# Kernel optimization log

Measured on AMD Instinct MI355X. Metric: run time of the kernel, lower is better.

## Reference

```python
import jax, jax.numpy as jnp
import numpy as np

B, N, D = 32, 64, 256

def _gelu(x):
    return jax.nn.gelu(x, approximate=False)

def setup_inputs() -> dict:
    key = jax.random.key(0)
    ks = jax.random.split(key, 16)
    def w(k, shape):
        fan_in = shape[0]
        return (jax.random.normal(k, shape, jnp.float32) / np.float32(np.sqrt(fan_in)))
    return {
        "dataset_embedding": jax.random.normal(ks[0], (B, D), jnp.float32),
        "variable_embeddings": jax.random.normal(ks[1], (B, N, D), jnp.float32),
        "claim_context": jax.random.normal(ks[2], (B, D), jnp.float32),
        "dge_w1": w(ks[3], (2 * D, D)), "dge_b1": jnp.zeros((D,), jnp.float32),
        "dge_w2": w(ks[4], (D, D)),     "dge_b2": jnp.zeros((D,), jnp.float32),
        "cge_w1": w(ks[5], (2 * D, D)), "cge_b1": jnp.zeros((D,), jnp.float32),
        "cge_w2": w(ks[6], (D, D)),     "cge_b2": jnp.zeros((D,), jnp.float32),
        "dep_w1": w(ks[7], (4 * D, D)), "dep_b1": jnp.zeros((D,), jnp.float32),
        "dep_w2": w(ks[8], (D, 1)),     "dep_b2": jnp.zeros((1,), jnp.float32),
        "cep_w1": w(ks[9], (4 * D, D)), "cep_b1": jnp.zeros((D,), jnp.float32),
        "cep_w2": w(ks[10], (D, 1)),    "cep_b2": jnp.zeros((1,), jnp.float32),
        "gate_w1": w(ks[11], (3, 64)),  "gate_b1": jnp.zeros((64,), jnp.float32),
        "gate_w2": w(ks[12], (64, 1)),  "gate_b2": jnp.zeros((1,), jnp.float32),
        "n_samples": 500,
    }

def _encode(ve, ctx, w1, b1, w2, b2):
    # Sequential(Linear(2d,d), GELU, Linear(d,d), GELU); dropout=0 (eval)
    x = jnp.concatenate([ve, jnp.broadcast_to(ctx[:, None, :], ve.shape)], axis=-1)
    h = _gelu(x @ w1 + b1)
    return _gelu(h @ w2 + b2)

def _predict_edges(ve_enc, ctx, w1, b1, w2, b2):
    # var_with_context: [B,N,2D]; edge features cat([var_i, var_j]) @ w1
    # == (vwc @ w1[:2D]) broadcast over i + (vwc @ w1[2D:]) broadcast over j
    vwc = jnp.concatenate([ve_enc, jnp.broadcast_to(ctx[:, None, :], ve_enc.shape)], axis=-1)
    wi, wj = w1[: 2 * D], w1[2 * D :]
    fi = vwc @ wi  # [B,N,D]
    fj = vwc @ wj  # [B,N,D]
    h = _gelu(fi[:, :, None, :] + fj[:, None, :, :] + b1)  # [B,N,N,D]
    logits = jnp.einsum("bijd,do->bij", h, w2) + b2[0]
    eye = jnp.eye(N, dtype=bool)
    return jnp.where(eye[None, :, :], jnp.float32(-1e9), logits)

def reference(dataset_embedding, variable_embeddings, claim_context,
              dge_w1, dge_b1, dge_w2, dge_b2,
              cge_w1, cge_b1, cge_w2, cge_b2,
              dep_w1, dep_b1, dep_w2, dep_b2,
              cep_w1, cep_b1, cep_w2, cep_b2,
              gate_w1, gate_b1, gate_w2, gate_b2,
              n_samples):
    avg_claim_confidence = 0.5
    var_data = _encode(variable_embeddings, dataset_embedding, dge_w1, dge_b1, dge_w2, dge_b2)
    var_claim = _encode(variable_embeddings, claim_context, cge_w1, cge_b1, cge_w2, cge_b2)
    W_data_logits = _predict_edges(var_data, dataset_embedding, dep_w1, dep_b1, dep_w2, dep_b2)
    W_claim_logits = _predict_edges(var_claim, claim_context, cep_w1, cep_b1, cep_w2, cep_b2)

    p = jax.nn.sigmoid(W_data_logits)
    eps = jnp.float32(1e-8)
    data_entropy = -(p * jnp.log(p + eps) + (1 - p) * jnp.log(1 - p + eps)).mean(axis=(1, 2))  # [B]

    ns = jnp.full((B,), min(n_samples / 1000.0, 1.0), jnp.float32)
    cc = jnp.full((B,), avg_claim_confidence, jnp.float32)
    gf = jnp.stack([ns, cc, data_entropy], axis=-1)  # [B,3]
    gate = jax.nn.sigmoid(_gelu(gf @ gate_w1 + gate_b1) @ gate_w2 + gate_b2)  # [B,1]
    gate = gate[:, :, None]  # [B,1,1]

    W_post_logits = gate * W_data_logits + (1 - gate) * W_claim_logits

    # NOTEARS: h(W) = tr(expm(W o W)) - n, W = sigmoid(logits)
    Wsig = jax.nn.sigmoid(W_post_logits)
    M = jax.vmap(jax.scipy.linalg.expm)(Wsig * Wsig)
    acyc = (jnp.trace(M, axis1=1, axis2=2) - N).mean()

    W_posterior = jax.nn.sigmoid(W_post_logits)
    return (W_posterior, acyc)
```

## Files before the change

### kernel.cpp

```cpp
#include <hip/hip_runtime.h>
#include <hip/hip_bf16.h>


#define LDS_STRIDE 260
#define ES 68

__device__ __forceinline__ float gelu_f(float x) {
    return 0.5f * x * (1.0f + erff(x * 0.70710678118654752440f));
}
__device__ __forceinline__ float sigmoid_f(float x) {
    return 1.0f / (1.0f + expf(-x));
}
__device__ __forceinline__ float f4c(const float4& v, int k) {
    return k == 0 ? v.x : k == 1 ? v.y : k == 2 ? v.z : v.w;
}
__device__ __forceinline__ float4 ld4(const float* __restrict__ buf, int r, int c) {
    return *(const float4*)&buf[r * ES + c];
}

__global__ __launch_bounds__(256) void k0_ctx(
    const float* __restrict__ ds, const float* __restrict__ cc,
    const float* __restrict__ dge_w1, const float* __restrict__ dge_b1,
    const float* __restrict__ cge_w1, const float* __restrict__ cge_b1,
    const float* __restrict__ dep_w1, const float* __restrict__ dep_b1,
    const float* __restrict__ cep_w1, const float* __restrict__ cep_b1,
    float* __restrict__ ctxproj)
{
    const int b = blockIdx.x;
    const int which = blockIdx.y;
    const float* ctx; const float* W; const float* bias;
    switch (which) {
        case 0:  ctx = ds; W = dge_w1 + 256 * 256; bias = dge_b1; break;
        case 1:  ctx = cc; W = cge_w1 + 256 * 256; bias = cge_b1; break;
        case 2:  ctx = ds; W = dep_w1 + 256 * 256; bias = dep_b1; break;
        case 3:  ctx = ds; W = dep_w1 + 768 * 256; bias = nullptr; break;
        case 4:  ctx = cc; W = cep_w1 + 256 * 256; bias = cep_b1; break;
        default: ctx = cc; W = cep_w1 + 768 * 256; bias = nullptr; break;
    }
    __shared__ float sctx[256];
    const int tid = threadIdx.x;
    sctx[tid] = ctx[b * 256 + tid];
    __syncthreads();
    float acc = 0.0f;
    #pragma unroll 2
    for (int k = 0; k < 256; k += 4) {
        float4 c4 = *(const float4*)&sctx[k];
        acc = fmaf(c4.x, W[(k + 0) * 256 + tid], acc);
        acc = fmaf(c4.y, W[(k + 1) * 256 + tid], acc);
        acc = fmaf(c4.z, W[(k + 2) * 256 + tid], acc);
        acc = fmaf(c4.w, W[(k + 3) * 256 + tid], acc);
    }
    if (bias) acc += bias[tid];
    ctxproj[(which * 32 + b) * 256 + tid] = acc;
}

__device__ __forceinline__ void gemm_ks(const float* __restrict__ src,
                                        const float* __restrict__ W,
                                        int ks0, int t0, float acc[8][4])
{
    #pragma unroll
    for (int r = 0; r < 8; ++r)
        #pragma unroll
        for (int c = 0; c < 4; ++c) acc[r][c] = 0.0f;
    #pragma unroll 2
    for (int k = ks0; k < ks0 + 32; k += 4) {
        float4 wv0 = *(const float4*)&W[(k + 0) * 256 + t0];
        float4 wv1 = *(const float4*)&W[(k + 1) * 256 + t0];
        float4 wv2 = *(const float4*)&W[(k + 2) * 256 + t0];
        float4 wv3 = *(const float4*)&W[(k + 3) * 256 + t0];
        float4 a[8];
        #pragma unroll
        for (int r = 0; r < 8; ++r) a[r] = *(const float4*)&src[r * LDS_STRIDE + k];
        float4 wvs[4] = {wv0, wv1, wv2, wv3};
        #pragma unroll
        for (int kk = 0; kk < 4; ++kk) {
            float4 wv = wvs[kk];
            #pragma unroll
            for (int r = 0; r < 8; ++r) {
                float av = f4c(a[r], kk);
                acc[r][0] = fmaf(av, wv.x, acc[r][0]);
                acc[r][1] = fmaf(av, wv.y, acc[r][1]);
                acc[r][2] = fmaf(av, wv.z, acc[r][2]);
                acc[r][3] = fmaf(av, wv.w, acc[r][3]);
            }
        }
    }
}

__device__ __forceinline__ void write_part(float* __restrict__ part, int w, int t0,
                                           const float acc[8][4])
{
    #pragma unroll
    for (int r = 0; r < 8; ++r) {
        float4 o = {acc[r][0], acc[r][1], acc[r][2], acc[r][3]};
        *(float4*)&part[(w * 8 + r) * 256 + t0] = o;
    }
}

__device__ __forceinline__ float4 reduce_part(const float* __restrict__ part, int r, int t0)
{
    float4 s = {0.0f, 0.0f, 0.0f, 0.0f};
    #pragma unroll
    for (int w = 0; w < 8; ++w) {
        float4 v = *(const float4*)&part[(w * 8 + r) * 256 + t0];
        s.x += v.x; s.y += v.y; s.z += v.z; s.w += v.w;
    }
    return s;
}

__global__ __launch_bounds__(512) void k1_encode(
    const float* __restrict__ ve_g,
    const float* __restrict__ dge_w1, const float* __restrict__ dge_w2, const float* __restrict__ dge_b2,
    const float* __restrict__ cge_w1, const float* __restrict__ cge_w2, const float* __restrict__ cge_b2,
    const float* __restrict__ dep_w1, const float* __restrict__ cep_w1,
    const float* __restrict__ ctxproj,
    float* __restrict__ fi_dep, float* __restrict__ fjt_dep,
    float* __restrict__ fi_cep, float* __restrict__ fjt_cep)
{
    __shared__ float sve[8 * LDS_STRIDE];
    __shared__ float sA[8 * LDS_STRIDE];
    __shared__ float sB[8 * LDS_STRIDE];
    __shared__ float part[8 * 8 * 256];

    const int tid = threadIdx.x;
    const int b = blockIdx.x >> 3;
    const int chunk = blockIdx.x & 7;
    const int n0 = chunk * 8;

    const int w  = tid >> 6;
    const int t0 = (tid & 63) * 4;
    const int ks0 = w * 32;

    {
        int idx = tid * 4;
        int r = idx >> 8, k = idx & 255;
        *(float4*)&sve[r * LDS_STRIDE + k] = *(const float4*)&ve_g[(b * 64 + n0) * 256 + idx];
    }
    __syncthreads();

    float acc[8][4];

    gemm_ks(sve, dge_w1, ks0, t0, acc);
    write_part(part, w, t0, acc);
    __syncthreads();
    {
        float4 s = reduce_part(part, w, t0);
        float4 cp = *(const float4*)&ctxproj[(0 * 32 + b) * 256 + t0];
        float4 o = {gelu_f(s.x + cp.x), gelu_f(s.y + cp.y), gelu_f(s.z + cp.z), gelu_f(s.w + cp.w)};
        *(float4*)&sA[w * LDS_STRIDE + t0] = o;
    }
    __syncthreads();

    gemm_ks(sA, dge_w2, ks0, t0, acc);
    write_part(part, w, t0, acc);
    __syncthreads();
    {
        float4 s = reduce_part(part, w, t0);
        float4 bv = *(const float4*)&dge_b2[t0];
        float4 o = {gelu_f(s.x + bv.x), gelu_f(s.y + bv.y), gelu_f(s.z + bv.z), gelu_f(s.w + bv.w)};
        *(float4*)&sB[w * LDS_STRIDE + t0] = o;
    }
    __syncthreads();

    gemm_ks(sB, dep_w1, ks0, t0, acc);
    write_part(part, w, t0, acc);
    __syncthreads();
    {
        float4 s = reduce_part(part, w, t0);
        float4 cp = *(const float4*)&ctxproj[(2 * 32 + b) * 256 + t0];
        float4 o = {s.x + cp.x, s.y + cp.y, s.z + cp.z, s.w + cp.w};
        *(float4*)&fi_dep[(b * 64 + n0 + w) * 256 + t0] = o;
    }
    __syncthreads();

    gemm_ks(sB, dep_w1 + 512 * 256, ks0, t0, acc);
    write_part(part, w, t0, acc);
    __syncthreads();
    {
        float4 s = reduce_part(part, w, t0);
        float4 cp = *(const float4*)&ctxproj[(3 * 32 + b) * 256 + t0];
        float4 o = {s.x + cp.x, s.y + cp.y, s.z + cp.z, s.w + cp.w};
        *(float4*)&sA[w * LDS_STRIDE + t0] = o;
    }
    __syncthreads();
    {
        int t = tid & 255, half = tid >> 8;
        float v0 = sA[(half * 4 + 0) * LDS_STRIDE + t];
        float v1 = sA[(half * 4 + 1) * LDS_STRIDE + t];
        float v2 = sA[(half * 4 + 2) * LDS_STRIDE + t];
        float v3 = sA[(half * 4 + 3) * LDS_STRIDE + t];
        float4 o = {v0, v1, v2, v3};
        *(float4*)&fjt_dep[(b * 256 + t) * 64 + n0 + half * 4] = o;
    }

    gemm_ks(sve, cge_w1, ks0, t0, acc);
    write_part(part, w, t0, acc);
    __syncthreads();
    {
        float4 s = reduce_part(part, w, t0);
        float4 cp = *(const float4*)&ctxproj[(1 * 32 + b) * 256 + t0];
        float4 o = {gelu_f(s.x + cp.x), gelu_f(s.y + cp.y), gelu_f(s.z + cp.z), gelu_f(s.w + cp.w)};
        *(float4*)&sB[w * LDS_STRIDE + t0] = o;
    }
    __syncthreads();

    gemm_ks(sB, cge_w2, ks0, t0, acc);
    write_part(part, w, t0, acc);
    __syncthreads();
    {
        float4 s = reduce_part(part, w, t0);
        float4 bv = *(const float4*)&cge_b2[t0];
        float4 o = {gelu_f(s.x + bv.x), gelu_f(s.y + bv.y), gelu_f(s.z + bv.z), gelu_f(s.w + bv.w)};
        *(float4*)&sA[w * LDS_STRIDE + t0] = o;
    }
    __syncthreads();

    gemm_ks(sA, cep_w1, ks0, t0, acc);
    write_part(part, w, t0, acc);
    __syncthreads();
    {
        float4 s = reduce_part(part, w, t0);
        float4 cp = *(const float4*)&ctxproj[(4 * 32 + b) * 256 + t0];
        float4 o = {s.x + cp.x, s.y + cp.y, s.z + cp.z, s.w + cp.w};
        *(float4*)&fi_cep[(b * 64 + n0 + w) * 256 + t0] = o;
    }
    __syncthreads();

    gemm_ks(sA, cep_w1 + 512 * 256, ks0, t0, acc);
    write_part(part, w, t0, acc);
    __syncthreads();
    {
        float4 s = reduce_part(part, w, t0);
        float4 cp = *(const float4*)&ctxproj[(5 * 32 + b) * 256 + t0];
        float4 o = {s.x + cp.x, s.y + cp.y, s.z + cp.z, s.w + cp.w};
        *(float4*)&sB[w * LDS_STRIDE + t0] = o;
    }
    __syncthreads();
    {
        int t = tid & 255, half = tid >> 8;
        float v0 = sB[(half * 4 + 0) * LDS_STRIDE + t];
        float v1 = sB[(half * 4 + 1) * LDS_STRIDE + t];
        float v2 = sB[(half * 4 + 2) * LDS_STRIDE + t];
        float v3 = sB[(half * 4 + 3) * LDS_STRIDE + t];
        float4 o = {v0, v1, v2, v3};
        *(float4*)&fjt_cep[(b * 256 + t) * 64 + n0 + half * 4] = o;
    }
}

__global__ __launch_bounds__(256) void k3_edges(
    const float* __restrict__ fi_dep, const float* __restrict__ fjt_dep,
    const float* __restrict__ fi_cep, const float* __restrict__ fjt_cep,
    const float* __restrict__ dep_w2, const float* __restrict__ dep_b2,
    const float* __restrict__ cep_w2, const float* __restrict__ cep_b2,
    float* __restrict__ Wd, float* __restrict__ Wc, float* __restrict__ entp)
{
    __shared__ float fjD_s[64 * 64];
    __shared__ float fjC_s[64 * 64];
    __shared__ float fiD_s[4][256];
    __shared__ float fiC_s[4][256];
    __shared__ float w2D_s[256];
    __shared__ float w2C_s[256];

    const int b   = blockIdx.x >> 4;
    const int ig  = blockIdx.x & 15;
    const int tid = threadIdx.x;
    const int s   = tid >> 6;
    const int j   = tid & 63;
    const int i   = ig * 4 + s;

    {
        int c = j * 4;
        *(float4*)&fiD_s[s][c] = *(const float4*)&fi_dep[(b * 64 + i) * 256 + c];
        *(float4*)&fiC_s[s][c] = *(const float4*)&fi_cep[(b * 64 + i) * 256 + c];
        if (tid < 64) {
            *(float4*)&w2D_s[tid * 4] = *(const float4*)&dep_w2[tid * 4];
        } else if (tid < 128) {
            int t = tid - 64;
            *(float4*)&w2C_s[t * 4] = *(const float4*)&cep_w2[t * 4];
        }
    }

    float accD0 = 0.0f, accD1 = 0.0f, accC0 = 0.0f, accC1 = 0.0f;

    for (int c0 = 0; c0 < 256; c0 += 64) {
        if (c0) __syncthreads();
        {
            const float4* sD = (const float4*)(fjt_dep + (b * 256 + c0) * 64);
            const float4* sC = (const float4*)(fjt_cep + (b * 256 + c0) * 64);
            #pragma unroll
            for (int kk = 0; kk < 4; ++kk) {
                ((float4*)fjD_s)[tid + kk * 256] = sD[tid + kk * 256];
                ((float4*)fjC_s)[tid + kk * 256] = sC[tid + kk * 256];
            }
        }
        __syncthreads();

        #pragma unroll 4
        for (int d = 0; d < 64; d += 2) {
            float fid0 = fiD_s[s][c0 + d];
            float fid1 = fiD_s[s][c0 + d + 1];
            float fic0 = fiC_s[s][c0 + d];
            float fic1 = fiC_s[s][c0 + d + 1];
            float fjd0 = fjD_s[(d + 0) * 64 + j];
            float fjd1 = fjD_s[(d + 1) * 64 + j];
            float fjc0 = fjC_s[(d + 0) * 64 + j];
            float fjc1 = fjC_s[(d + 1) * 64 + j];
            float wd0 = w2D_s[c0 + d], wd1 = w2D_s[c0 + d + 1];
            float wc0 = w2C_s[c0 + d], wc1 = w2C_s[c0 + d + 1];
            accD0 = fmaf(gelu_f(fid0 + fjd0), wd0, accD0);
            accD1 = fmaf(gelu_f(fid1 + fjd1), wd1, accD1);
            accC0 = fmaf(gelu_f(fic0 + fjc0), wc0, accC0);
            accC1 = fmaf(gelu_f(fic1 + fjc1), wc1, accC1);
        }
    }

    float lD = (accD0 + accD1) + dep_b2[0];
    float lC = (accC0 + accC1) + cep_b2[0];
    if (j == i) { lD = -1e9f; lC = -1e9f; }
    Wd[(b * 64 + i) * 64 + j] = lD;
    Wc[(b * 64 + i) * 64 + j] = lC;

    float p = sigmoid_f(lD);
    float e = -(p * logf(p + 1e-8f) + (1.0f - p) * logf(1.0f - p + 1e-8f));
    #pragma unroll
    for (int off = 32; off; off >>= 1) e += __shfl_down(e, off);
    if (j == 0) entp[b * 64 + i] = e;
}

__device__ __forceinline__ void mm64f(const float* __restrict__ A, const float* __restrict__ B,
                                      int r0, int c0, float acc[4][4])
{
    #pragma unroll
    for (int i = 0; i < 4; ++i)
        #pragma unroll
        for (int j = 0; j < 4; ++j) acc[i][j] = 0.0f;
    for (int kb = 0; kb < 64; kb += 4) {
        float4 xa[4];
        #pragma unroll
        for (int i = 0; i < 4; ++i) xa[i] = ld4(A, r0 + i, kb);
        #pragma unroll
        for (int kk = 0; kk < 4; ++kk) {
            float4 rv = ld4(B, kb + kk, c0);
            float rj[4] = {rv.x, rv.y, rv.z, rv.w};
            #pragma unroll
            for (int i = 0; i < 4; ++i) {
                float xv = f4c(xa[i], kk);
                #pragma unroll
                for (int j = 0; j < 4; ++j) acc[i][j] = fmaf(xv, rj[j], acc[i][j]);
            }
        }
    }
}

__device__ __forceinline__ void mm64d(const float* __restrict__ A, const float* __restrict__ B,
                                      int r0, int c0, double acc[4][4])
{
    #pragma unroll
    for (int i = 0; i < 4; ++i)
        #pragma unroll
        for (int j = 0; j < 4; ++j) acc[i][j] = 0.0;
    for (int kb = 0; kb < 64; kb += 4) {
        float4 xa[4];
        #pragma unroll
        for (int i = 0; i < 4; ++i) xa[i] = ld4(A, r0 + i, kb);
        #pragma unroll
        for (int kk = 0; kk < 4; ++kk) {
            float4 rv = ld4(B, kb + kk, c0);
            double rj[4] = {(double)rv.x, (double)rv.y, (double)rv.z, (double)rv.w};
            #pragma unroll
            for (int i = 0; i < 4; ++i) {
                double xv = (double)f4c(xa[i], kk);
                #pragma unroll
                for (int j = 0; j < 4; ++j) acc[i][j] = fma(xv, rj[j], acc[i][j]);
            }
        }
    }
}

__global__ __launch_bounds__(256) void k6_gate_expm(
    const float* __restrict__ Wd, const float* __restrict__ Wc,
    const float* __restrict__ entp,
    const float* __restrict__ gw1, const float* __restrict__ gb1,
    const float* __restrict__ gw2, const float* __restrict__ gb2,
    const int* __restrict__ n_samples,
    float* __restrict__ out, float* __restrict__ traces)
{
    __shared__ float Xs [64 * ES];
    __shared__ float X2s[64 * ES];
    __shared__ float X3s[64 * ES];
    __shared__ float Ra [64 * ES];
    __shared__ float Rb [64 * ES];
    __shared__ float sgate;
    __shared__ float sent;
    __shared__ int ssexp;

    const int b = blockIdx.x;
    const int tid = threadIdx.x;

    const float C2 = 0.5f, C3 = 1.0f/6.0f, C4 = 1.0f/24.0f, C5 = 1.0f/120.0f;
    const float C6 = 1.0f/720.0f, C7 = 1.0f/5040.0f, C8 = 1.0f/40320.0f;
    const float C9 = 1.0f/362880.0f, C10 = 1.0f/3628800.0f, C11 = 1.0f/39916800.0f;
    const float C12 = 1.0f/479001600.0f, C13 = 1.0f/6227020800.0f;

    if (tid == 0) {
        float s = 0.0f;
        for (int c = 0; c < 64; ++c) s += entp[b * 64 + c];
        sent = s / 4096.0f;
    }
    __syncthreads();
    if (tid < 64) {
        float ns = fminf((float)n_samples[0] / 1000.0f, 1.0f);
        float ccf = 0.5f;
        float pre = ns * gw1[tid] + ccf * gw1[64 + tid] + sent * gw1[128 + tid] + gb1[tid];
        float hid = gelu_f(pre) * gw2[tid];
        #pragma unroll
        for (int off = 32; off; off >>= 1) hid += __shfl_down(hid, off);
        if (tid == 0) sgate = sigmoid_f(hid + gb2[0]);
    }
    __syncthreads();
    const float g = sgate;

    for (int idx = tid; idx < 4096; idx += 256) {
        float d = Wd[b * 4096 + idx];
        float c = Wc[b * 4096 + idx];
        float post = g * d + (1.0f - g) * c;
        float sg = sigmoid_f(post);
        out[b * 4096 + idx] = sg;
        Xs[(idx >> 6) * ES + (idx & 63)] = sg * sg;
    }
    __syncthreads();

    if (tid < 64) {
        float cs = 0.0f;
        for (int r = 0; r < 64; ++r) cs += Xs[r * ES + tid];
        #pragma unroll
        for (int off = 32; off; off >>= 1) cs = fmaxf(cs, __shfl_down(cs, off));
        if (tid == 0) {
            int se = 0;
            if (cs > 1.0f) se = (int)ceilf(log2f(cs));
            if (se < 0) se = 0;
            if (se > 12) se = 12;
            ssexp = se;
        }
    }
    __syncthreads();
    const int sexp = ssexp;
    const float scale = ldexpf(1.0f, -sexp);
    for (int idx = tid; idx < 4096; idx += 256) {
        Xs[(idx >> 6) * ES + (idx & 63)] *= scale;
    }
    __syncthreads();

    const int rq = tid >> 4, cq = tid & 15;
    const int r0 = rq * 4, c0 = cq * 4;
    float acc[4][4];

    mm64f(Xs, Xs, r0, c0, acc);
    #pragma unroll
    for (int i = 0; i < 4; ++i) {
        float4 o = {acc[i][0], acc[i][1], acc[i][2], acc[i][3]};
        *(float4*)&X2s[(r0 + i) * ES + c0] = o;
    }
    __syncthreads();

    mm64f(X2s, Xs, r0, c0, acc);
    #pragma unroll
    for (int i = 0; i < 4; ++i) {
        float4 o = {acc[i][0], acc[i][1], acc[i][2], acc[i][3]};
        *(float4*)&X3s[(r0 + i) * ES + c0] = o;
    }
    __syncthreads();

    mm64f(Xs, X3s, r0, c0, acc);
    #pragma unroll
    for (int i = 0; i < 4; ++i) {
        float4 xv = ld4(Xs, r0 + i, c0);
        float4 x2 = ld4(X2s, r0 + i, c0);
        float4 x3 = ld4(X3s, r0 + i, c0);
        float o[4];
        #pragma unroll
        for (int j = 0; j < 4; ++j) {
            o[j] = C13 * acc[i][j] + C12 * f4c(x3, j) + C10 * f4c(xv, j) + C11 * f4c(x2, j)
                 + ((r0 + i) == (c0 + j) ? C9 : 0.0f);
        }
        float4 ov = {o[0], o[1], o[2], o[3]};
        *(float4*)&Ra[(r0 + i) * ES + c0] = ov;
    }
    __syncthreads();

    mm64f(Ra, X3s, r0, c0, acc);
    #pragma unroll
    for (int i = 0; i < 4; ++i) {
        float4 xv = ld4(Xs, r0 + i, c0);
        float4 x2 = ld4(X2s, r0 + i, c0);
        float o[4];
        #pragma unroll
        for (int j = 0; j < 4; ++j) {
            o[j] = acc[i][j] + C7 * f4c(xv, j) + C8 * f4c(x2, j)
                 + ((r0 + i) == (c0 + j) ? C6 : 0.0f);
        }
        float4 ov = {o[0], o[1], o[2], o[3]};
        *(float4*)&Rb[(r0 + i) * ES + c0] = ov;
    }
    __syncthreads();

    mm64f(Rb, X3s, r0, c0, acc);
    #pragma unroll
    for (int i = 0; i < 4; ++i) {
        float4 xv = ld4(Xs, r0 + i, c0);
        float4 x2 = ld4(X2s, r0 + i, c0);
        float o[4];
        #pragma unroll
        for (int j = 0; j < 4; ++j) {
            o[j] = acc[i][j] + C4 * f4c(xv, j) + C5 * f4c(x2, j)
                 + ((r0 + i) == (c0 + j) ? C3 : 0.0f);
        }
        float4 ov = {o[0], o[1], o[2], o[3]};
        *(float4*)&Ra[(r0 + i) * ES + c0] = ov;
    }
    __syncthreads();

    mm64f(Ra, X3s, r0, c0, acc);
    #pragma unroll
    for (int i = 0; i < 4; ++i) {
        float4 xv = ld4(Xs, r0 + i, c0);
        float4 x2 = ld4(X2s, r0 + i, c0);
        float o[4];
        #pragma unroll
        for (int j = 0; j < 4; ++j) {
            o[j] = acc[i][j] + f4c(xv, j) + C2 * f4c(x2, j)
                 + ((r0 + i) == (c0 + j) ? 1.0f : 0.0f);
        }
        float4 ov = {o[0], o[1], o[2], o[3]};
        *(float4*)&Rb[(r0 + i) * ES + c0] = ov;
    }
    __syncthreads();

    float* cur = Rb;
    float* oth = Ra;
    for (int sq = 0; sq < sexp; ++sq) {
        double dacc[4][4];
        mm64d(cur, cur, r0, c0, dacc);
        #pragma unroll
        for (int i = 0; i < 4; ++i) {
            float4 o = {(float)dacc[i][0], (float)dacc[i][1], (float)dacc[i][2], (float)dacc[i][3]};
            *(float4*)&oth[(r0 + i) * ES + c0] = o;
        }
        __syncthreads();
        float* t = cur; cur = oth; oth = t;
    }

    if (tid == 0) {
        double tr = 0.0;
        for (int i = 0; i < 64; ++i) tr += (double)cur[i * ES + i];
        traces[b] = (float)tr;
    }
}

__global__ void k7_acyc(const float* __restrict__ traces, float* __restrict__ out)
{
    if (threadIdx.x == 0 && blockIdx.x == 0) {
        double s = 0.0;
        for (int b = 0; b < 32; ++b) s += (double)traces[b];
        out[131072] = (float)(s / 32.0 - 64.0);
    }
}

extern "C" void kernel_launch(void* const* d_in, const int* in_sizes, int n_in,
                              void* d_out, int out_size, void* d_ws, size_t ws_size,
                              hipStream_t stream)
{
    (void)in_sizes; (void)n_in; (void)out_size; (void)ws_size;

    const float* ds     = (const float*)d_in[0];
    const float* ve     = (const float*)d_in[1];
    const float* cc     = (const float*)d_in[2];
    const float* dge_w1 = (const float*)d_in[3];
    const float* dge_b1 = (const float*)d_in[4];
    const float* dge_w2 = (const float*)d_in[5];
    const float* dge_b2 = (const float*)d_in[6];
    const float* cge_w1 = (const float*)d_in[7];
    const float* cge_b1 = (const float*)d_in[8];
    const float* cge_w2 = (const float*)d_in[9];
    const float* cge_b2 = (const float*)d_in[10];
    const float* dep_w1 = (const float*)d_in[11];
    const float* dep_b1 = (const float*)d_in[12];
    const float* dep_w2 = (const float*)d_in[13];
    const float* dep_b2 = (const float*)d_in[14];
    const float* cep_w1 = (const float*)d_in[15];
    const float* cep_b1 = (const float*)d_in[16];
    const float* cep_w2 = (const float*)d_in[17];
    const float* cep_b2 = (const float*)d_in[18];
    const float* gw1    = (const float*)d_in[19];
    const float* gb1    = (const float*)d_in[20];
    const float* gw2    = (const float*)d_in[21];
    const float* gb2    = (const float*)d_in[22];
    const int*   nsamp  = (const int*)d_in[23];

    float* ws = (float*)d_ws;
    float* ctxproj = ws;
    float* fi_dep  = ctxproj + 49152;
    float* fjt_dep = fi_dep + 524288;
    float* fi_cep  = fjt_dep + 524288;
    float* fjt_cep = fi_cep + 524288;
    float* Wd      = fjt_cep + 524288;
    float* Wc      = Wd + 131072;
    float* entp    = Wc + 131072;
    float* traces  = entp + 2048;

    float* outp = (float*)d_out;

    k0_ctx<<<dim3(32, 6), 256, 0, stream>>>(ds, cc, dge_w1, dge_b1, cge_w1, cge_b1,
                                            dep_w1, dep_b1, cep_w1, cep_b1, ctxproj);
    k1_encode<<<256, 512, 0, stream>>>(ve, dge_w1, dge_w2, dge_b2,
                                       cge_w1, cge_w2, cge_b2,
                                       dep_w1, cep_w1, ctxproj,
                                       fi_dep, fjt_dep, fi_cep, fjt_cep);
    k3_edges<<<512, 256, 0, stream>>>(fi_dep, fjt_dep, fi_cep, fjt_cep,
                                      dep_w2, dep_b2, cep_w2, cep_b2,
                                      Wd, Wc, entp);
    k6_gate_expm<<<32, 256, 0, stream>>>(Wd, Wc, entp, gw1, gb1, gw2, gb2,
                                         nsamp, outp, traces);
    k7_acyc<<<1, 64, 0, stream>>>(traces, outp);
}
```

Baseline: 136.6 us.

## Use polynomial erf approximation in GELU and split edge reduction across 512 threads

```diff
diff --git a/kernel.cpp b/kernel.cpp
--- a/kernel.cpp
+++ b/kernel.cpp
@@ -6,7 +6,14 @@
 #define ES 68
 
 __device__ __forceinline__ float gelu_f(float x) {
-    return 0.5f * x * (1.0f + erff(x * 0.70710678118654752440f));
+    float z = fabsf(x) * 0.70710678118654752440f;
+    float t = 1.0f / fmaf(0.3275911f, z, 1.0f);
+    float p = t * fmaf(t, fmaf(t, fmaf(t, fmaf(t, 1.061405429f, -1.453152027f),
+                                       1.421413741f), -0.284496736f), 0.254829592f);
+    float e = __expf(-z * z);
+    float erfv = fmaf(-p, e, 1.0f);
+    erfv = copysignf(erfv, x);
+    return 0.5f * x * (1.0f + erfv);
 }
 __device__ __forceinline__ float sigmoid_f(float x) {
     return 1.0f / (1.0f + expf(-x));
@@ -247,7 +254,7 @@
     }
 }
 
-__global__ __launch_bounds__(256) void k3_edges(
+__global__ __launch_bounds__(512) void k3_edges(
     const float* __restrict__ fi_dep, const float* __restrict__ fjt_dep,
     const float* __restrict__ fi_cep, const float* __restrict__ fjt_cep,
     const float* __restrict__ dep_w2, const float* __restrict__ dep_b2,
@@ -260,71 +267,84 @@
     __shared__ float fiC_s[4][256];
     __shared__ float w2D_s[256];
     __shared__ float w2C_s[256];
+    __shared__ float redD[8][64];
+    __shared__ float redC[8][64];
 
     const int b   = blockIdx.x >> 4;
     const int ig  = blockIdx.x & 15;
     const int tid = threadIdx.x;
     const int s   = tid >> 6;
     const int j   = tid & 63;
-    const int i   = ig * 4 + s;
-
-    {
-        int c = j * 4;
-        *(float4*)&fiD_s[s][c] = *(const float4*)&fi_dep[(b * 64 + i) * 256 + c];
-        *(float4*)&fiC_s[s][c] = *(const float4*)&fi_cep[(b * 64 + i) * 256 + c];
-        if (tid < 64) {
-            *(float4*)&w2D_s[tid * 4] = *(const float4*)&dep_w2[tid * 4];
-        } else if (tid < 128) {
-            int t = tid - 64;
-            *(float4*)&w2C_s[t * 4] = *(const float4*)&cep_w2[t * 4];
-        }
-    }
-
-    float accD0 = 0.0f, accD1 = 0.0f, accC0 = 0.0f, accC1 = 0.0f;
+    const int row = s & 3;
+    const int dh  = s >> 2;
+
+    if (tid < 256) {
+        int rr = tid >> 6, c = (tid & 63) * 4;
+        *(float4*)&fiD_s[rr][c] = *(const float4*)&fi_dep[(b * 64 + ig * 4 + rr) * 256 + c];
+    } else {
+        int t2 = tid - 256;
+        int rr = t2 >> 6, c = (t2 & 63) * 4;
+        *(float4*)&fiC_s[rr][c] = *(const float4*)&fi_cep[(b * 64 + ig * 4 + rr) * 256 + c];
+    }
+    if (tid < 64) {
+        *(float4*)&w2D_s[tid * 4] = *(const float4*)&dep_w2[tid * 4];
+    } else if (tid < 128) {
+        int t = tid - 64;
+        *(float4*)&w2C_s[t * 4] = *(const float4*)&cep_w2[t * 4];
+    }
+
+    float accD = 0.0f, accC = 0.0f;
 
     for (int c0 = 0; c0 < 256; c0 += 64) {
         if (c0) __syncthreads();
         {
             const float4* sD = (const float4*)(fjt_dep + (b * 256 + c0) * 64);
             const float4* sC = (const float4*)(fjt_cep + (b * 256 + c0) * 64);
-            #pragma unroll
-            for (int kk = 0; kk < 4; ++kk) {
-                ((float4*)fjD_s)[tid + kk * 256] = sD[tid + kk * 256];
-                ((float4*)fjC_s)[tid + kk * 256] = sC[tid + kk * 256];
-            }
+            ((float4*)fjD_s)[tid]       = sD[tid];
+            ((float4*)fjD_s)[tid + 512] = sD[tid + 512];
+            ((float4*)fjC_s)[tid]       = sC[tid];
+            ((float4*)fjC_s)[tid + 512] = sC[tid + 512];
         }
         __syncthreads();
 
+        const int d0 = dh * 32;
         #pragma unroll 4
-        for (int d = 0; d < 64; d += 2) {
-            float fid0 = fiD_s[s][c0 + d];
-            float fid1 = fiD_s[s][c0 + d + 1];
-            float fic0 = fiC_s[s][c0 + d];
-            float fic1 = fiC_s[s][c0 + d + 1];
+        for (int d = d0; d < d0 + 32; d += 2) {
+            float fid0 = fiD_s[row][c0 + d];
+            float fid1 = fiD_s[row][c0 + d + 1];
+            float fic0 = fiC_s[row][c0 + d];
+            float fic1 = fiC_s[row][c0 + d + 1];
             float fjd0 = fjD_s[(d + 0) * 64 + j];
             float fjd1 = fjD_s[(d + 1) * 64 + j];
             float fjc0 = fjC_s[(d + 0) * 64 + j];
             float fjc1 = fjC_s[(d + 1) * 64 + j];
             float wd0 = w2D_s[c0 + d], wd1 = w2D_s[c0 + d + 1];
             float wc0 = w2C_s[c0 + d], wc1 = w2C_s[c0 + d + 1];
-            accD0 = fmaf(gelu_f(fid0 + fjd0), wd0, accD0);
-            accD1 = fmaf(gelu_f(fid1 + fjd1), wd1, accD1);
-            accC0 = fmaf(gelu_f(fic0 + fjc0), wc0, accC0);
-            accC1 = fmaf(gelu_f(fic1 + fjc1), wc1, accC1);
-        }
-    }
-
-    float lD = (accD0 + accD1) + dep_b2[0];
-    float lC = (accC0 + accC1) + cep_b2[0];
-    if (j == i) { lD = -1e9f; lC = -1e9f; }
-    Wd[(b * 64 + i) * 64 + j] = lD;
-    Wc[(b * 64 + i) * 64 + j] = lC;
-
-    float p = sigmoid_f(lD);
-    float e = -(p * logf(p + 1e-8f) + (1.0f - p) * logf(1.0f - p + 1e-8f));
-    #pragma unroll
-    for (int off = 32; off; off >>= 1) e += __shfl_down(e, off);
-    if (j == 0) entp[b * 64 + i] = e;
+            accD = fmaf(gelu_f(fid0 + fjd0), wd0, accD);
+            accD = fmaf(gelu_f(fid1 + fjd1), wd1, accD);
+            accC = fmaf(gelu_f(fic0 + fjc0), wc0, accC);
+            accC = fmaf(gelu_f(fic1 + fjc1), wc1, accC);
+        }
+    }
+
+    redD[s][j] = accD;
+    redC[s][j] = accC;
+    __syncthreads();
+
+    if (s < 4) {
+        const int i = ig * 4 + s;
+        float lD = (redD[s][j] + redD[s + 4][j]) + dep_b2[0];
+        float lC = (redC[s][j] + redC[s + 4][j]) + cep_b2[0];
+        if (j == i) { lD = -1e9f; lC = -1e9f; }
+        Wd[(b * 64 + i) * 64 + j] = lD;
+        Wc[(b * 64 + i) * 64 + j] = lC;
+
+        float p = sigmoid_f(lD);
+        float e = -(p * logf(p + 1e-8f) + (1.0f - p) * logf(1.0f - p + 1e-8f));
+        #pragma unroll
+        for (int off = 32; off; off >>= 1) e += __shfl_down(e, off);
+        if (j == 0) entp[b * 64 + i] = e;
+    }
 }
 
 __device__ __forceinline__ void mm64f(const float* __restrict__ A, const float* __restrict__ B,
@@ -616,7 +636,7 @@
                                        cge_w1, cge_w2, cge_b2,
                                        dep_w1, cep_w1, ctxproj,
                                        fi_dep, fjt_dep, fi_cep, fjt_cep);
-    k3_edges<<<512, 256, 0, stream>>>(fi_dep, fjt_dep, fi_cep, fjt_cep,
+    k3_edges<<<512, 512, 0, stream>>>(fi_dep, fjt_dep, fi_cep, fjt_cep,
                                       dep_w2, dep_b2, cep_w2, cep_b2,
                                       Wd, Wc, entp);
     k6_gate_expm<<<32, 256, 0, stream>>>(Wd, Wc, entp, gw1, gb1, gw2, gb2,
```

Result: slower. 144.8 us (+6.0%).
